# Optimization experiments

Hardware: AMD Instinct MI355X
Metric: run time of the kernel (lower is better)

Reference implementation:

```python
import jax, jax.numpy as jnp
import numpy as np


def setup_inputs() -> dict:
    key = jax.random.key(0)
    ks = jax.random.split(key, 10)
    B, S, V, E, C = 256, 512, 50000, 300, 10
    sentences = jax.random.randint(ks[0], (B, S), 0, V)
    emb_table = jax.random.normal(ks[1], (V, E), dtype=jnp.float32) * 0.1
    # pad_token=0 row zeroed like nn.Embedding(padding_idx=0)
    emb_table = emb_table.at[0].set(0.0)
    k3 = jax.random.normal(ks[2], (3, E), dtype=jnp.float32) * 0.05
    b3 = jax.random.normal(ks[3], (1,), dtype=jnp.float32) * 0.05
    k4 = jax.random.normal(ks[4], (4, E), dtype=jnp.float32) * 0.05
    b4 = jax.random.normal(ks[5], (1,), dtype=jnp.float32) * 0.05
    k5 = jax.random.normal(ks[6], (5, E), dtype=jnp.float32) * 0.05
    b5 = jax.random.normal(ks[7], (1,), dtype=jnp.float32) * 0.05
    fc_w = jax.random.normal(ks[8], (C, 3), dtype=jnp.float32) * 0.1
    fc_b = jax.random.normal(ks[9], (C,), dtype=jnp.float32) * 0.1
    return {"sentences": sentences, "emb_table": emb_table,
            "k3": k3, "b3": b3, "k4": k4, "b4": b4, "k5": k5, "b5": b5,
            "fc_w": fc_w, "fc_b": fc_b}


def _window_feature(emb, k, b):
    # emb: [B,S,E]; k: [w,E]; conv with 1 in/1 out channel spanning full E (VALID)
    out = jax.lax.conv_general_dilated(
        emb[:, None, :, :],            # [B,1,S,E]
        k[None, None, :, :],           # [1,1,w,E]
        window_strides=(1, 1), padding="VALID")  # [B,1,S-w+1,1]
    f = jnp.tanh(out[:, 0, :, 0] + b)  # [B,S-w+1]
    return f.max(axis=-1)              # [B]


def reference(sentences, emb_table, k3, b3, k4, b4, k5, b5, fc_w, fc_b):
    emb = emb_table[sentences]  # [B,S,E]
    feats = jnp.stack([_window_feature(emb, k3, b3),
                       _window_feature(emb, k4, b4),
                       _window_feature(emb, k5, b5)], axis=-1)  # [B,3]
    # dropout is identity in eval mode
    logits = feats @ fc_w.T + fc_b  # [B,C]
    return jax.nn.log_softmax(logits, axis=-1)
```

## Files before the change

kernel.cpp:

```cpp
#include <hip/hip_runtime.h>
#include <hip/hip_bf16.h>
#include <math.h>

#define NSENT 256
#define SLEN  512
#define VROWS 50000
#define EDIM  300
#define NROW  12
#define NSTEP 10

typedef __attribute__((ext_vector_type(8))) short bf16x8;
typedef __attribute__((ext_vector_type(4))) float f32x4;

static __device__ __forceinline__ short f2bf(float f) {
    __hip_bfloat16 h = __float2bfloat16(f);
    short s;
    __builtin_memcpy(&s, &h, sizeof(s));
    return s;
}

__global__ __launch_bounds__(256, 2)
void vocab_scores_mfma(const float* __restrict__ emb,
                       const float* __restrict__ k3,
                       const float* __restrict__ k4,
                       const float* __restrict__ k5,
                       float* __restrict__ s)
{
    const int lane = threadIdx.x & 63;
    const int wave = threadIdx.x >> 6;
    const int rc   = lane & 15;
    const int kg   = lane >> 4;

    const int vbase = blockIdx.x * 64 + wave * 16;
    const int vrow  = min(vbase + rc, VROWS - 1);

    const float* krow = nullptr;
    if      (rc < 3)  krow = k3 + rc * EDIM;
    else if (rc < 7)  krow = k4 + (rc - 3) * EDIM;
    else if (rc < 12) krow = k5 + (rc - 7) * EDIM;

    bf16x8 bfrag[NSTEP];
    #pragma unroll
    for (int st = 0; st < NSTEP; ++st) {
        const int k0 = st * 32 + kg * 8;
        float4 b0 = make_float4(0.f,0.f,0.f,0.f);
        float4 b1 = make_float4(0.f,0.f,0.f,0.f);
        if (krow) {
            if (k0 + 4 <= EDIM) b0 = *reinterpret_cast<const float4*>(krow + k0);
            if (k0 + 8 <= EDIM) b1 = *reinterpret_cast<const float4*>(krow + k0 + 4);
        }
        bf16x8 f;
        f[0]=f2bf(b0.x); f[1]=f2bf(b0.y); f[2]=f2bf(b0.z); f[3]=f2bf(b0.w);
        f[4]=f2bf(b1.x); f[5]=f2bf(b1.y); f[6]=f2bf(b1.z); f[7]=f2bf(b1.w);
        bfrag[st] = f;
    }

    const float* arow = emb + (size_t)vrow * EDIM;
    float4 a0[NSTEP], a1[NSTEP];
    #pragma unroll
    for (int st = 0; st < NSTEP; ++st) {
        const int k0 = st * 32 + kg * 8;
        a0[st] = (k0 + 4 <= EDIM) ? *reinterpret_cast<const float4*>(arow + k0)
                                  : make_float4(0.f,0.f,0.f,0.f);
        a1[st] = (k0 + 8 <= EDIM) ? *reinterpret_cast<const float4*>(arow + k0 + 4)
                                  : make_float4(0.f,0.f,0.f,0.f);
    }

    f32x4 acc = {0.f, 0.f, 0.f, 0.f};
    #pragma unroll
    for (int st = 0; st < NSTEP; ++st) {
        bf16x8 af;
        af[0]=f2bf(a0[st].x); af[1]=f2bf(a0[st].y);
        af[2]=f2bf(a0[st].z); af[3]=f2bf(a0[st].w);
        af[4]=f2bf(a1[st].x); af[5]=f2bf(a1[st].y);
        af[6]=f2bf(a1[st].z); af[7]=f2bf(a1[st].w);
        acc = __builtin_amdgcn_mfma_f32_16x16x32_bf16(af, bfrag[st], acc, 0, 0, 0);
    }

    if (rc < NROW) {
        #pragma unroll
        for (int j = 0; j < 4; ++j) {
            const int v = vbase + kg * 4 + j;
            if (v < VROWS) s[(size_t)v * NROW + rc] = acc[j];
        }
    }
}

__global__ __launch_bounds__(1024, 1)
void textcnn_finish(const int*   __restrict__ sent,
                    const float* __restrict__ s,
                    const float* __restrict__ b3,
                    const float* __restrict__ b4,
                    const float* __restrict__ b5,
                    const float* __restrict__ fcw,
                    const float* __restrict__ fcb,
                    float* __restrict__ out)
{
    __shared__ float s_lds[NROW * SLEN];
    __shared__ float red[8][3];

    const int b = blockIdx.x;
    const int t = threadIdx.x;

    auto gather = [&](int token, int j) {
        const int widx = sent[b * SLEN + token];
        const float4 v = reinterpret_cast<const float4*>(s + (size_t)widx * NROW)[j];
        s_lds[(4*j + 0) * SLEN + token] = v.x;
        s_lds[(4*j + 1) * SLEN + token] = v.y;
        s_lds[(4*j + 2) * SLEN + token] = v.z;
        s_lds[(4*j + 3) * SLEN + token] = v.w;
    };

    gather(t & 511, t >> 9);
    if (t < SLEN) gather(t, 2);
    __syncthreads();

    if (t < SLEN) {
        const float bb3 = b3[0], bb4 = b4[0], bb5 = b5[0];
        float m3 = -1e30f, m4 = -1e30f, m5 = -1e30f;
        if (t < SLEN - 2)
            m3 = tanhf(s_lds[0*SLEN + t] + s_lds[1*SLEN + t+1] +
                       s_lds[2*SLEN + t+2] + bb3);
        if (t < SLEN - 3)
            m4 = tanhf(s_lds[3*SLEN + t] + s_lds[4*SLEN + t+1] +
                       s_lds[5*SLEN + t+2] + s_lds[6*SLEN + t+3] + bb4);
        if (t < SLEN - 4)
            m5 = tanhf(s_lds[7*SLEN + t] + s_lds[8*SLEN + t+1] +
                       s_lds[9*SLEN + t+2] + s_lds[10*SLEN + t+3] +
                       s_lds[11*SLEN + t+4] + bb5);

        #pragma unroll
        for (int off = 32; off; off >>= 1) {
            m3 = fmaxf(m3, __shfl_xor(m3, off));
            m4 = fmaxf(m4, __shfl_xor(m4, off));
            m5 = fmaxf(m5, __shfl_xor(m5, off));
        }
        if ((t & 63) == 0) {
            const int w = t >> 6;
            red[w][0] = m3; red[w][1] = m4; red[w][2] = m5;
        }
    }
    __syncthreads();

    if (t == 0) {
        float f3 = red[0][0], f4 = red[0][1], f5 = red[0][2];
        #pragma unroll
        for (int w = 1; w < 8; ++w) {
            f3 = fmaxf(f3, red[w][0]);
            f4 = fmaxf(f4, red[w][1]);
            f5 = fmaxf(f5, red[w][2]);
        }
        float lg[10];
        float mx = -1e30f;
        #pragma unroll
        for (int c = 0; c < 10; ++c) {
            lg[c] = fcb[c] + f3 * fcw[c*3+0] + f4 * fcw[c*3+1] + f5 * fcw[c*3+2];
            mx = fmaxf(mx, lg[c]);
        }
        float ssum = 0.f;
        #pragma unroll
        for (int c = 0; c < 10; ++c) ssum += expf(lg[c] - mx);
        const float lse = logf(ssum);
        #pragma unroll
        for (int c = 0; c < 10; ++c) out[b * 10 + c] = lg[c] - mx - lse;
    }
}

extern "C" void kernel_launch(void* const* d_in, const int* in_sizes, int n_in,
                              void* d_out, int out_size, void* d_ws, size_t ws_size,
                              hipStream_t stream) {
    const int*   sent = (const int*)  d_in[0];
    const float* emb  = (const float*)d_in[1];
    const float* k3   = (const float*)d_in[2];
    const float* b3   = (const float*)d_in[3];
    const float* k4   = (const float*)d_in[4];
    const float* b4   = (const float*)d_in[5];
    const float* k5   = (const float*)d_in[6];
    const float* b5   = (const float*)d_in[7];
    const float* fcw  = (const float*)d_in[8];
    const float* fcb  = (const float*)d_in[9];
    float* out = (float*)d_out;
    float* s   = (float*)d_ws;

    const int nblk = (VROWS + 63) / 64;
    vocab_scores_mfma<<<nblk, 256, 0, stream>>>(emb, k3, k4, k5, s);
    textcnn_finish<<<NSENT, 1024, 0, stream>>>(sent, s, b3, b4, b5, fcw, fcb, out);
}
```

Baseline: 28.98 us.

## Stage weight fragments in LDS and split A loads to cut registers

Weight B-fragments are now built once per block, cooperatively across all 256 threads, and stored in shared memory, where before every wave rebuilt them in registers. Embedding-row loads are split into two halves of five steps, so only half of the A data sits in registers at once. Launch bounds rise to 4 blocks per SM, aiming for more waves in flight to hide global memory latency in this bandwidth-bound vocab pass. The costs are a __syncthreads, LDS reads on every MFMA step, and less load-level parallelism per thread.

```diff
diff --git a/kernel.cpp b/kernel.cpp
--- a/kernel.cpp
+++ b/kernel.cpp
@@ -19,30 +19,31 @@
     return s;
 }
 
-__global__ __launch_bounds__(256, 2)
+__global__ __launch_bounds__(256, 4)
 void vocab_scores_mfma(const float* __restrict__ emb,
                        const float* __restrict__ k3,
                        const float* __restrict__ k4,
                        const float* __restrict__ k5,
                        float* __restrict__ s)
 {
-    const int lane = threadIdx.x & 63;
-    const int wave = threadIdx.x >> 6;
+    __shared__ bf16x8 bfrag_lds[NSTEP * 64];
+
+    const int tid  = threadIdx.x;
+    const int lane = tid & 63;
+    const int wave = tid >> 6;
     const int rc   = lane & 15;
     const int kg   = lane >> 4;
 
-    const int vbase = blockIdx.x * 64 + wave * 16;
-    const int vrow  = min(vbase + rc, VROWS - 1);
-
-    const float* krow = nullptr;
-    if      (rc < 3)  krow = k3 + rc * EDIM;
-    else if (rc < 7)  krow = k4 + (rc - 3) * EDIM;
-    else if (rc < 12) krow = k5 + (rc - 7) * EDIM;
-
-    bf16x8 bfrag[NSTEP];
-    #pragma unroll
-    for (int st = 0; st < NSTEP; ++st) {
-        const int k0 = st * 32 + kg * 8;
+    for (int e = tid; e < NSTEP * 64; e += 256) {
+        const int st  = e >> 6;
+        const int le  = e & 63;
+        const int rce = le & 15;
+        const int kge = le >> 4;
+        const float* krow = nullptr;
+        if      (rce < 3)  krow = k3 + rce * EDIM;
+        else if (rce < 7)  krow = k4 + (rce - 3) * EDIM;
+        else if (rce < 12) krow = k5 + (rce - 7) * EDIM;
+        const int k0 = st * 32 + kge * 8;
         float4 b0 = make_float4(0.f,0.f,0.f,0.f);
         float4 b1 = make_float4(0.f,0.f,0.f,0.f);
         if (krow) {
@@ -52,29 +53,40 @@
         bf16x8 f;
         f[0]=f2bf(b0.x); f[1]=f2bf(b0.y); f[2]=f2bf(b0.z); f[3]=f2bf(b0.w);
         f[4]=f2bf(b1.x); f[5]=f2bf(b1.y); f[6]=f2bf(b1.z); f[7]=f2bf(b1.w);
-        bfrag[st] = f;
-    }
-
+        bfrag_lds[e] = f;
+    }
+    __syncthreads();
+
+    const int vbase = blockIdx.x * 64 + wave * 16;
+    const int vrow  = min(vbase + rc, VROWS - 1);
     const float* arow = emb + (size_t)vrow * EDIM;
-    float4 a0[NSTEP], a1[NSTEP];
+
+    f32x4 acc = {0.f, 0.f, 0.f, 0.f};
+
     #pragma unroll
-    for (int st = 0; st < NSTEP; ++st) {
-        const int k0 = st * 32 + kg * 8;
-        a0[st] = (k0 + 4 <= EDIM) ? *reinterpret_cast<const float4*>(arow + k0)
-                                  : make_float4(0.f,0.f,0.f,0.f);
-        a1[st] = (k0 + 8 <= EDIM) ? *reinterpret_cast<const float4*>(arow + k0 + 4)
-                                  : make_float4(0.f,0.f,0.f,0.f);
-    }
-
-    f32x4 acc = {0.f, 0.f, 0.f, 0.f};
-    #pragma unroll
-    for (int st = 0; st < NSTEP; ++st) {
-        bf16x8 af;
-        af[0]=f2bf(a0[st].x); af[1]=f2bf(a0[st].y);
-        af[2]=f2bf(a0[st].z); af[3]=f2bf(a0[st].w);
-        af[4]=f2bf(a1[st].x); af[5]=f2bf(a1[st].y);
-        af[6]=f2bf(a1[st].z); af[7]=f2bf(a1[st].w);
-        acc = __builtin_amdgcn_mfma_f32_16x16x32_bf16(af, bfrag[st], acc, 0, 0, 0);
+    for (int half = 0; half < 2; ++half) {
+        float4 a0[5], a1[5];
+        #pragma unroll
+        for (int i = 0; i < 5; ++i) {
+            const int k0 = (half * 5 + i) * 32 + kg * 8;
+            a0[i] = (k0 + 4 <= EDIM)
+                  ? *reinterpret_cast<const float4*>(arow + k0)
+                  : make_float4(0.f,0.f,0.f,0.f);
+            a1[i] = (k0 + 8 <= EDIM)
+                  ? *reinterpret_cast<const float4*>(arow + k0 + 4)
+                  : make_float4(0.f,0.f,0.f,0.f);
+        }
+        #pragma unroll
+        for (int i = 0; i < 5; ++i) {
+            const int st = half * 5 + i;
+            const bf16x8 bf = bfrag_lds[st * 64 + lane];
+            bf16x8 af;
+            af[0]=f2bf(a0[i].x); af[1]=f2bf(a0[i].y);
+            af[2]=f2bf(a0[i].z); af[3]=f2bf(a0[i].w);
+            af[4]=f2bf(a1[i].x); af[5]=f2bf(a1[i].y);
+            af[6]=f2bf(a1[i].z); af[7]=f2bf(a1[i].w);
+            acc = __builtin_amdgcn_mfma_f32_16x16x32_bf16(af, bf, acc, 0, 0, 0);
+        }
     }
 
     if (rc < NROW) {
```

Result: faster. 24.57 us (-15.2%).
